# Optimization experiments

Measured on AMD Instinct MI355X. Metric: run time of the kernel, lower is better.

## Reference

```python
import jax, jax.numpy as jnp
import numpy as np

N = 100000; EI = 1600000; EC = 800000; G = 2000
FD = 512; H1 = 32; H2 = 32; EMB = 128; NH = 4
EPS = 1e-5


def setup_inputs() -> dict:
    key = jax.random.key(0)
    ks = jax.random.split(key, 30)
    p = lambda k, shp: (jax.random.normal(k, shp, jnp.float32) * 0.05)
    inp = {
        'feat': jax.random.normal(ks[0], (N, FD), jnp.float32),
        'inter_src': jax.random.randint(ks[1], (EI,), 0, N),
        'inter_dst': jax.random.randint(ks[2], (EI,), 0, N),
        'cross_src': jax.random.randint(ks[3], (EC,), 0, N),
        'cross_dst': jax.random.randint(ks[4], (EC,), 0, N),
        'graph_ids': jnp.sort(jax.random.randint(ks[5], (N,), 0, G)),
        # layer1
        'W_gc1': p(ks[6], (FD, NH * H1)), 'b_gc1': p(ks[7], (NH * H1,)),
        'W_gat1': p(ks[8], (FD, NH * H1)), 'al1': p(ks[9], (NH, H1)), 'ar1': p(ks[10], (NH, H1)), 'b_gat1': p(ks[11], (NH * H1,)),
        # layer2
        'W_gc2': p(ks[12], (NH * H1, NH * H2)), 'b_gc2': p(ks[13], (NH * H2,)),
        'W_gat2': p(ks[14], (NH * H1, NH * H2)), 'al2': p(ks[15], (NH, H2)), 'ar2': p(ks[16], (NH, H2)), 'b_gat2': p(ks[17], (NH * H2,)),
        # layer3
        'W_gc3': p(ks[18], (NH * H2, EMB)), 'b_gc3': p(ks[19], (EMB,)),
        'W_gat3': p(ks[20], (NH * H2, EMB)), 'al3': p(ks[21], (1, EMB)), 'ar3': p(ks[22], (1, EMB)), 'b_gat3': p(ks[23], (EMB,)),
        # batchnorms (gamma ones, beta zeros)
        'g1': jnp.ones((NH * H1,), jnp.float32), 'be1': jnp.zeros((NH * H1,), jnp.float32),
        'g2': jnp.ones((NH * H2,), jnp.float32), 'be2': jnp.zeros((NH * H2,), jnp.float32),
        'g3': jnp.ones((EMB,), jnp.float32), 'be3': jnp.zeros((EMB,), jnp.float32),
    }
    return inp


def _leaky(x):
    return jnp.where(x >= 0, x, 0.2 * x)


def _graph_conv(x, W, b, src, dst):
    # DGL GraphConv, norm='both': D_out^{-1/2} A D_in^{-1/2} X W + b (degrees clamped to >=1)
    ones = jnp.ones(src.shape[0], x.dtype)
    dout = jnp.clip(jax.ops.segment_sum(ones, src, num_segments=N), 1.0)
    din = jnp.clip(jax.ops.segment_sum(ones, dst, num_segments=N), 1.0)
    xw = (x @ W) * (dout ** -0.5)[:, None]          # project first (in >= out)
    agg = jax.ops.segment_sum(xw[src], dst, num_segments=N)
    return agg * (din ** -0.5)[:, None] + b


def _gat(x, W, al, ar, b, src, dst, H, d):
    # DGL GATConv: per-edge additive attention with edge softmax over incoming edges
    f = (x @ W).reshape(-1, H, d)                    # [N,H,d]
    el = jnp.sum(f * al, -1)                         # [N,H]
    er = jnp.sum(f * ar, -1)
    e = _leaky(el[src] + er[dst])                    # [E,H]
    m = jax.ops.segment_max(e, dst, num_segments=N)
    ex = jnp.exp(e - m[dst])
    s = jax.ops.segment_sum(ex, dst, num_segments=N)
    alpha = ex / s[dst]                              # [E,H]
    out = jax.ops.segment_sum(alpha[:, :, None] * f[src], dst, num_segments=N)
    return out + b.reshape(1, H, d), alpha


def _bn(x, g, b):
    mu = x.mean(0)
    v = jnp.mean((x - mu) ** 2, 0)
    return g * (x - mu) / jnp.sqrt(v + EPS) + b


def reference(feat, inter_src, inter_dst, cross_src, cross_dst, graph_ids,
              W_gc1, b_gc1, W_gat1, al1, ar1, b_gat1,
              W_gc2, b_gc2, W_gat2, al2, ar2, b_gat2,
              W_gc3, b_gc3, W_gat3, al3, ar3, b_gat3,
              g1, be1, g2, be2, g3, be3):
    h = feat
    hi = _graph_conv(h, W_gc1, b_gc1, inter_src, inter_dst)
    hc, _ = _gat(h, W_gat1, al1, ar1, b_gat1, cross_src, cross_dst, NH, H1)
    h = _bn(_leaky(hi + hc.reshape(N, -1)), g1, be1)
    hi = _graph_conv(h, W_gc2, b_gc2, inter_src, inter_dst)
    hc, _ = _gat(h, W_gat2, al2, ar2, b_gat2, cross_src, cross_dst, NH, H2)
    h = _bn(_leaky(hi + hc.reshape(N, -1)), g2, be2)
    h1 = _graph_conv(h, W_gc3, b_gc3, inter_src, inter_dst)
    h2, att = _gat(h, W_gat3, al3, ar3, b_gat3, cross_src, cross_dst, 1, EMB)
    h = _bn(h1 + h2[:, 0, :], g3, be3)
    att_sum = jax.ops.segment_sum(att[:, 0], cross_src, num_segments=N)   # [N]
    wh = h * att_sum[:, None]
    gsum = jax.ops.segment_sum(wh, graph_ids, num_segments=G)
    cnt = jnp.clip(jax.ops.segment_sum(jnp.ones(N, h.dtype), graph_ids, num_segments=G), 1.0)
    frag_embeddings = gsum / cnt[:, None]                                  # [G,EMB]
    return frag_embeddings, att_sum
```

## Files before the change

### kernel.cpp

```cpp
#include <hip/hip_runtime.h>
#include <math.h>

#define NN 100000
#define EIE 1600000
#define ECE 800000
#define GG 2000
#define FDIM 512
#define CC 128
#define BNEPS 1e-5f
#define SLOTI 48
#define SLOTC 32
#define FUSED_BLOCKS 3910

static inline int cdiv(long a, long b){ return (int)((a+b-1)/b); }

typedef __attribute__((ext_vector_type(8))) short short8;
typedef __attribute__((ext_vector_type(4))) float f32x4;

__device__ __forceinline__ unsigned short f2bf(float f){
  unsigned u = __float_as_uint(f);
  u += 0x7fffu + ((u >> 16) & 1u);
  return (unsigned short)(u >> 16);
}
__device__ __forceinline__ float bf2f(unsigned short h){
  return __uint_as_float(((unsigned)h) << 16);
}
__device__ __forceinline__ float2 ldbf2(const unsigned short* p){
  ushort2 u = *(const ushort2*)p;
  return make_float2(bf2f(u.x), bf2f(u.y));
}

__device__ __forceinline__ size_t wt_off(int n, int k) {
  return (size_t)(k >> 5)*8192 + (((n >> 4)*4 + ((k >> 3) & 3))*16 + (n & 15))*8 + (k & 7);
}
__global__ void k_pack_all(const float* __restrict__ Wgc1, const float* __restrict__ Wgat1,
                           const float* __restrict__ Wgc2, const float* __restrict__ Wgat2,
                           const float* __restrict__ Wgc3, const float* __restrict__ Wgat3,
                           unsigned short* __restrict__ Wth1, unsigned short* __restrict__ Wtl1,
                           unsigned short* __restrict__ Wth2, unsigned short* __restrict__ Wtl2,
                           unsigned short* __restrict__ Wth3, unsigned short* __restrict__ Wtl3) {
  int t = blockIdx.x*256 + threadIdx.x;
  const float *W1, *W2; unsigned short *oh, *ol; int FIN, tt;
  if (t < 131072)      { W1=Wgc1; W2=Wgat1; oh=Wth1; ol=Wtl1; FIN=512; tt=t; }
  else if (t < 163840) { W1=Wgc2; W2=Wgat2; oh=Wth2; ol=Wtl2; FIN=128; tt=t-131072; }
  else if (t < 196608) { W1=Wgc3; W2=Wgat3; oh=Wth3; ol=Wtl3; FIN=128; tt=t-163840; }
  else return;
  int n = tt / FIN, k = tt % FIN;
  float v = (n < 128) ? W1[(size_t)k*128 + n] : W2[(size_t)k*128 + (n-128)];
  unsigned short h = f2bf(v);
  size_t o = wt_off(n, k);
  oh[o] = h;
  ol[o] = f2bf(v - bf2f(h));
}

__global__ __launch_bounds__(512)
void k_fill_gemm1(const int* __restrict__ isrc, const int* __restrict__ idst,
                  const int* __restrict__ csrc, const int* __restrict__ cdst,
                  int* __restrict__ cnt_i, int* __restrict__ eid_i,
                  int* __restrict__ cnt_c, int* __restrict__ eid_c,
                  int* __restrict__ dout, float* __restrict__ att,
                  const float* __restrict__ xf,
                  const unsigned short* __restrict__ Bh, const unsigned short* __restrict__ Bl,
                  const float* __restrict__ al, const float* __restrict__ ar,
                  float* __restrict__ el, float* __restrict__ er,
                  unsigned short* __restrict__ Y1, unsigned short* __restrict__ Y2) {
  __shared__ __attribute__((aligned(16))) unsigned short sAh[4096];
  __shared__ __attribute__((aligned(16))) unsigned short sBh[8192];
  __shared__ __attribute__((aligned(16))) unsigned short sBl[8192];
  int r = blockIdx.x;
  int tid = threadIdx.x;

  if (r % 5 != 0) {
    int fi = r - 1 - (r-1)/5;
    int e = fi*512 + tid;
    if (e < EIE) {
      int d = idst[e];
      int p = atomicAdd(&cnt_i[d], 1);
      if (p < SLOTI) eid_i[d*SLOTI + p] = isrc[e];
      atomicAdd(&dout[isrc[e]], 1);
    }
    if (e < ECE) {
      int d = cdst[e];
      int p = atomicAdd(&cnt_c[d], 1);
      if (p < SLOTC) eid_c[d*SLOTC + p] = csrc[e];
    }
    if (e < NN) att[e] = 0.f;
    return;
  }

  int row0 = (r/5)*128;
  int lane = tid & 63, wid = tid >> 6;
  int wm = wid >> 2, wn = wid & 3;
  int l15 = lane & 15, quad = lane >> 4;

  f32x4 acc[4][4];
  #pragma unroll
  for (int mt = 0; mt < 4; ++mt)
    #pragma unroll
    for (int nt = 0; nt < 4; ++nt) acc[mt][nt] = (f32x4){0.f,0.f,0.f,0.f};

  for (int k0 = 0; k0 < FDIM; k0 += 32) {
    #pragma unroll
    for (int i = 0; i < 2; ++i) {
      int idx = tid + i*512;
      int rr = idx >> 3, c = idx & 7;
      int gr = row0 + rr; if (gr > NN-1) gr = NN-1;
      float4 v = *(const float4*)(xf + (size_t)gr*FDIM + k0 + c*4);
      ushort4 hh;
      hh.x = f2bf(v.x); hh.y = f2bf(v.y); hh.z = f2bf(v.z); hh.w = f2bf(v.w);
      *(ushort4*)&sAh[(((rr>>4)*4 + (c>>1))*16 + (rr&15))*8 + (c&1)*4] = hh;
    }
    const unsigned short* bhk = Bh + (size_t)k0*256;
    const unsigned short* blk = Bl + (size_t)k0*256;
    #pragma unroll
    for (int i = 0; i < 2; ++i) {
      int idx = tid + i*512;
      *(float4*)&sBh[idx*8] = *(const float4*)(bhk + idx*8);
      *(float4*)&sBl[idx*8] = *(const float4*)(blk + idx*8);
    }
    __syncthreads();
    short8 ah[4];
    #pragma unroll
    for (int mt = 0; mt < 4; ++mt)
      ah[mt] = *(const short8*)&sAh[(((wm*4+mt)*4 + quad)*16 + l15)*8];
    #pragma unroll
    for (int nt = 0; nt < 4; ++nt) {
      int off = (((wn*4+nt)*4 + quad)*16 + l15)*8;
      short8 bh = *(const short8*)&sBh[off];
      short8 bl = *(const short8*)&sBl[off];
      #pragma unroll
      for (int mt = 0; mt < 4; ++mt) {
        acc[mt][nt] = __builtin_amdgcn_mfma_f32_16x16x32_bf16(ah[mt], bh, acc[mt][nt], 0,0,0);
        acc[mt][nt] = __builtin_amdgcn_mfma_f32_16x16x32_bf16(ah[mt], bl, acc[mt][nt], 0,0,0);
      }
    }
    __syncthreads();
  }
  unsigned short* Y = (wn < 2) ? Y1 : Y2;
  int colbase = (wn & 1)*64;
  #pragma unroll
  for (int mt = 0; mt < 4; ++mt) {
    #pragma unroll
    for (int rr = 0; rr < 4; ++rr) {
      int row = row0 + (wm*4+mt)*16 + quad*4 + rr;
      if (row >= NN) continue;
      #pragma unroll
      for (int nt = 0; nt < 4; ++nt)
        Y[(size_t)row*CC + colbase + nt*16 + l15] = f2bf(acc[mt][nt][rr]);
    }
  }
  if (wn >= 2) {
    float alv[4], arv[4];
    #pragma unroll
    for (int nt = 0; nt < 4; ++nt) {
      int col = colbase + nt*16 + l15;
      alv[nt] = al[col]; arv[nt] = ar[col];
    }
    int hb = (wn & 1)*2;
    #pragma unroll
    for (int mt = 0; mt < 4; ++mt) {
      #pragma unroll
      for (int rr = 0; rr < 4; ++rr) {
        float pa0 = acc[mt][0][rr]*alv[0] + acc[mt][1][rr]*alv[1];
        float pb0 = acc[mt][0][rr]*arv[0] + acc[mt][1][rr]*arv[1];
        float pa1 = acc[mt][2][rr]*alv[2] + acc[mt][3][rr]*alv[3];
        float pb1 = acc[mt][2][rr]*arv[2] + acc[mt][3][rr]*arv[3];
        #pragma unroll
        for (int m = 1; m <= 8; m <<= 1) {
          pa0 += __shfl_xor(pa0, m); pb0 += __shfl_xor(pb0, m);
          pa1 += __shfl_xor(pa1, m); pb1 += __shfl_xor(pb1, m);
        }
        int row = row0 + (wm*4+mt)*16 + quad*4 + rr;
        if (l15 == 0 && row < NN) {
          el[(size_t)row*4 + hb]   = pa0;  er[(size_t)row*4 + hb]   = pb0;
          el[(size_t)row*4 + hb+1] = pa1;  er[(size_t)row*4 + hb+1] = pb1;
        }
      }
    }
  }
}

template<bool ELR>
__global__ __launch_bounds__(512)
void k_gemm2(const unsigned short* __restrict__ xb,
             const unsigned short* __restrict__ Bh, const unsigned short* __restrict__ Bl,
             const float* __restrict__ bnsc, const float* __restrict__ bnsh,
             const float* __restrict__ al, const float* __restrict__ ar,
             float* __restrict__ el, float* __restrict__ er,
             unsigned short* __restrict__ Y1, unsigned short* __restrict__ Y2) {
  __shared__ __attribute__((aligned(16))) unsigned short sAh[4096];
  __shared__ __attribute__((aligned(16))) unsigned short sBh[8192];
  __shared__ __attribute__((aligned(16))) unsigned short sBl[8192];
  int tid = threadIdx.x;
  int row0 = blockIdx.x*128;
  int lane = tid & 63, wid = tid >> 6;
  int wm = wid >> 2, wn = wid & 3;
  int l15 = lane & 15, quad = lane >> 4;

  f32x4 acc[4][4];
  #pragma unroll
  for (int mt = 0; mt < 4; ++mt)
    #pragma unroll
    for (int nt = 0; nt < 4; ++nt) acc[mt][nt] = (f32x4){0.f,0.f,0.f,0.f};

  for (int k0 = 0; k0 < CC; k0 += 32) {
    int rr = tid >> 2, c16 = tid & 3;
    int gr = row0 + rr; if (gr > NN-1) gr = NN-1;
    short8 u = *(const short8*)(xb + (size_t)gr*CC + k0 + c16*8);
    short8 o;
    #pragma unroll
    for (int j = 0; j < 8; ++j) {
      float f = bf2f((unsigned short)u[j]);
      f = f*bnsc[k0 + c16*8 + j] + bnsh[k0 + c16*8 + j];
      o[j] = (short)f2bf(f);
    }
    *(short8*)&sAh[(((rr>>4)*4 + c16)*16 + (rr&15))*8] = o;

    const unsigned short* bhk = Bh + (size_t)k0*256;
    const unsigned short* blk = Bl + (size_t)k0*256;
    #pragma unroll
    for (int i = 0; i < 2; ++i) {
      int idx = tid + i*512;
      *(float4*)&sBh[idx*8] = *(const float4*)(bhk + idx*8);
      *(float4*)&sBl[idx*8] = *(const float4*)(blk + idx*8);
    }
    __syncthreads();
    short8 ah[4];
    #pragma unroll
    for (int mt = 0; mt < 4; ++mt)
      ah[mt] = *(const short8*)&sAh[(((wm*4+mt)*4 + quad)*16 + l15)*8];
    #pragma unroll
    for (int nt = 0; nt < 4; ++nt) {
      int off = (((wn*4+nt)*4 + quad)*16 + l15)*8;
      short8 bh = *(const short8*)&sBh[off];
      short8 bl = *(const short8*)&sBl[off];
      #pragma unroll
      for (int mt = 0; mt < 4; ++mt) {
        acc[mt][nt] = __builtin_amdgcn_mfma_f32_16x16x32_bf16(ah[mt], bh, acc[mt][nt], 0,0,0);
        acc[mt][nt] = __builtin_amdgcn_mfma_f32_16x16x32_bf16(ah[mt], bl, acc[mt][nt], 0,0,0);
      }
    }
    __syncthreads();
  }
  unsigned short* Y = (wn < 2) ? Y1 : Y2;
  int colbase = (wn & 1)*64;
  #pragma unroll
  for (int mt = 0; mt < 4; ++mt) {
    #pragma unroll
    for (int rr = 0; rr < 4; ++rr) {
      int row = row0 + (wm*4+mt)*16 + quad*4 + rr;
      if (row >= NN) continue;
      #pragma unroll
      for (int nt = 0; nt < 4; ++nt)
        Y[(size_t)row*CC + colbase + nt*16 + l15] = f2bf(acc[mt][nt][rr]);
    }
  }
  if (ELR && wn >= 2) {
    float alv[4], arv[4];
    #pragma unroll
    for (int nt = 0; nt < 4; ++nt) {
      int col = colbase + nt*16 + l15;
      alv[nt] = al[col]; arv[nt] = ar[col];
    }
    int hb = (wn & 1)*2;
    #pragma unroll
    for (int mt = 0; mt < 4; ++mt) {
      #pragma unroll
      for (int rr = 0; rr < 4; ++rr) {
        float pa0 = acc[mt][0][rr]*alv[0] + acc[mt][1][rr]*alv[1];
        float pb0 = acc[mt][0][rr]*arv[0] + acc[mt][1][rr]*arv[1];
        float pa1 = acc[mt][2][rr]*alv[2] + acc[mt][3][rr]*alv[3];
        float pb1 = acc[mt][2][rr]*arv[2] + acc[mt][3][rr]*arv[3];
        #pragma unroll
        for (int m = 1; m <= 8; m <<= 1) {
          pa0 += __shfl_xor(pa0, m); pb0 += __shfl_xor(pb0, m);
          pa1 += __shfl_xor(pa1, m); pb1 += __shfl_xor(pb1, m);
        }
        int row = row0 + (wm*4+mt)*16 + quad*4 + rr;
        if (l15 == 0 && row < NN) {
          el[(size_t)row*4 + hb]   = pa0;  er[(size_t)row*4 + hb]   = pb0;
          el[(size_t)row*4 + hb+1] = pa1;  er[(size_t)row*4 + hb+1] = pb1;
        }
      }
    }
  }
}

template<int H>
__global__ __launch_bounds__(256)
void k_elr2(const unsigned short* __restrict__ f, const float* __restrict__ al,
            const float* __restrict__ ar, float* __restrict__ el, float* __restrict__ er,
            float* __restrict__ csq) {
  if (blockIdx.x == 0) csq[threadIdx.x] = 0.f;
  int lane = threadIdx.x & 63;
  int n = blockIdx.x*4 + (threadIdx.x >> 6);
  if (n >= NN) return;
  int c2 = lane*2;
  float2 v = ldbf2(f + (size_t)n*CC + c2);
  float2 a = *(const float2*)(al + c2);
  float2 b = *(const float2*)(ar + c2);
  float pa = v.x*a.x + v.y*a.y;
  float pb = v.x*b.x + v.y*b.y;
  const int W = (H == 1) ? 64 : 16;
  #pragma unroll
  for (int m = W>>1; m >= 1; m >>= 1) { pa += __shfl_xor(pa, m); pb += __shfl_xor(pb, m); }
  if ((lane & (W-1)) == 0) {
    int h = lane / W;
    el[(size_t)n*H + h] = pa;
    er[(size_t)n*H + h] = pb;
  }
}

template<int H, bool ATT, bool LEAKY>
__global__ __launch_bounds__(64)
void k_gather_fused(const unsigned short* __restrict__ A1, const unsigned short* __restrict__ A2,
                    const int* __restrict__ cnt_i, const int* __restrict__ eid_i,
                    const int* __restrict__ cnt_c, const int* __restrict__ eid_c,
                    const int* __restrict__ dout,
                    const float* __restrict__ el, const float* __restrict__ er,
                    const float* __restrict__ bgc, const float* __restrict__ bgat,
                    unsigned short* __restrict__ out, float* __restrict__ att) {
  int lane = threadIdx.x;
  int row = blockIdx.x;
  int grp = lane >> 4;
  int l4  = lane & 15;
  int c8  = l4*8;

  int deg = cnt_i[row];
  int lo = row*SLOTI, hi = lo + min(deg, SLOTI);
  float ax[8];
  #pragma unroll
  for (int k = 0; k < 8; ++k) ax[k] = 0.f;
  int j = lo + grp;
  for (; j + 4 < hi; j += 8) {
    int s0 = eid_i[j], s1 = eid_i[j+4];
    float d0 = rsqrtf((float)max(dout[s0], 1));
    float d1 = rsqrtf((float)max(dout[s1], 1));
    short8 u0 = *(const short8*)(A1 + (size_t)s0*CC + c8);
    short8 u1 = *(const short8*)(A1 + (size_t)s1*CC + c8);
    #pragma unroll
    for (int k = 0; k < 8; ++k)
      ax[k] += d0*bf2f((unsigned short)u0[k]) + d1*bf2f((unsigned short)u1[k]);
  }
  if (j < hi) {
    int s0 = eid_i[j];
    float d0 = rsqrtf((float)max(dout[s0], 1));
    short8 u0 = *(const short8*)(A1 + (size_t)s0*CC + c8);
    #pragma unroll
    for (int k = 0; k < 8; ++k) ax[k] += d0*bf2f((unsigned short)u0[k]);
  }
  float sc = rsqrtf((float)max(deg, 1));

  int h = (H == 1) ? 0 : (l4 >> 2);
  float erd = er[(size_t)row*H + h];
  int degc = cnt_c[row];
  int lo2 = row*SLOTC, hi2 = lo2 + min(degc, SLOTC);
  float gacc[8];
  #pragma unroll
  for (int k = 0; k < 8; ++k) gacc[k] = 0.f;
  float denom = 0.f;
  j = lo2 + grp;
  for (; j + 4 < hi2; j += 8) {
    int s0 = eid_c[j], s1 = eid_c[j+4];
    float v0 = el[(size_t)s0*H + h] + erd;
    float v1 = el[(size_t)s1*H + h] + erd;
    v0 = (v0 >= 0.f) ? v0 : 0.2f*v0;
    v1 = (v1 >= 0.f) ? v1 : 0.2f*v1;
    float w0 = __expf(v0), w1 = __expf(v1);
    denom += w0 + w1;
    short8 u0 = *(const short8*)(A2 + (size_t)s0*CC + c8);
    short8 u1 = *(const short8*)(A2 + (size_t)s1*CC + c8);
    #pragma unroll
    for (int k = 0; k < 8; ++k)
      gacc[k] += w0*bf2f((unsigned short)u0[k]) + w1*bf2f((unsigned short)u1[k]);
  }
  if (j < hi2) {
    int s = eid_c[j];
    float v = el[(size_t)s*H + h] + erd;
    v = (v >= 0.f) ? v : 0.2f*v;
    float w = __expf(v);
    denom += w;
    short8 u = *(const short8*)(A2 + (size_t)s*CC + c8);
    #pragma unroll
    for (int k = 0; k < 8; ++k) gacc[k] += w * bf2f((unsigned short)u[k]);
  }

  #pragma unroll
  for (int m = 16; m <= 32; m <<= 1) {
    denom += __shfl_xor(denom, m);
    #pragma unroll
    for (int k = 0; k < 8; ++k) {
      ax[k]   += __shfl_xor(ax[k], m);
      gacc[k] += __shfl_xor(gacc[k], m);
    }
  }
  float inv = (denom > 0.f) ? 1.0f/denom : 0.f;

  if (ATT) {
    for (j = lo2 + grp; j < hi2; j += 4) {
      int s = eid_c[j];
      if (l4 == 0) {
        float v = el[(size_t)s*H] + erd;
        v = (v >= 0.f) ? v : 0.2f*v;
        atomicAdd(&att[s], __expf(v)*inv);
      }
    }
  }

  if (grp == 0) {
    float4 b1a = *(const float4*)(bgc + c8);
    float4 b1b = *(const float4*)(bgc + c8 + 4);
    float4 b2a = *(const float4*)(bgat + c8);
    float4 b2b = *(const float4*)(bgat + c8 + 4);
    float bb1[8] = {b1a.x,b1a.y,b1a.z,b1a.w,b1b.x,b1b.y,b1b.z,b1b.w};
    float bb2[8] = {b2a.x,b2a.y,b2a.z,b2a.w,b2b.x,b2b.y,b2b.z,b2b.w};
    short8 ov;
    #pragma unroll
    for (int k = 0; k < 8; ++k) {
      float o = ax[k]*sc + bb1[k] + gacc[k]*inv + bb2[k];
      if (LEAKY) o = (o >= 0.f) ? o : 0.2f*o;
      ov[k] = (short)f2bf(o);
    }
    *(short8*)(out + (size_t)row*CC + c8) = ov;
  }
}

__global__ __launch_bounds__(256)
void k_bn_stats(const unsigned short* __restrict__ t, float* __restrict__ csq) {
  __shared__ float red[4][128];
  int lane = threadIdx.x & 63, g = threadIdx.x >> 6;
  int c2 = lane*2;
  float s0=0.f, s1=0.f, q0=0.f, q1=0.f;
  for (int r = blockIdx.x*4 + g; r < NN; r += gridDim.x*4) {
    float2 v = ldbf2(t + (size_t)r*CC + c2);
    s0 += v.x; s1 += v.y; q0 += v.x*v.x; q1 += v.y*v.y;
  }
  red[g][c2] = s0; red[g][c2+1] = s1;
  __syncthreads();
  if (threadIdx.x < 128) {
    float a = red[0][threadIdx.x] + red[1][threadIdx.x] + red[2][threadIdx.x] + red[3][threadIdx.x];
    atomicAdd(&csq[threadIdx.x], a);
  }
  __syncthreads();
  red[g][c2] = q0; red[g][c2+1] = q1;
  __syncthreads();
  if (threadIdx.x < 128) {
    float a = red[0][threadIdx.x] + red[1][threadIdx.x] + red[2][threadIdx.x] + red[3][threadIdx.x];
    atomicAdd(&csq[128 + threadIdx.x], a);
  }
}

__global__ void k_bn_coef(const float* __restrict__ csqc, float* __restrict__ csq,
                          const float* __restrict__ g, const float* __restrict__ be,
                          float* __restrict__ sc, float* __restrict__ sh) {
  int c = threadIdx.x;
  float sv = csqc[c], qv = csqc[128+c];
  float mu = sv * (1.f/NN);
  float var = qv * (1.f/NN) - mu*mu;
  float r = rsqrtf(var + BNEPS);
  float s = g[c]*r;
  sc[c] = s;
  sh[c] = be[c] - s*mu;
  csq[c] = 0.f; csq[128+c] = 0.f;
}

__global__ void k_pool_bn(const unsigned short* __restrict__ t, const float* __restrict__ att,
                          const int* __restrict__ gids, const float* __restrict__ bnsc,
                          const float* __restrict__ bnsh, float* __restrict__ frag) {
  int g = blockIdx.x;
  __shared__ int se[2];
  if (threadIdx.x < 2) {
    int target = g + threadIdx.x;
    int lo = 0, hi = NN;
    while (lo < hi) { int mid = (lo + hi) >> 1; if (gids[mid] < target) lo = mid + 1; else hi = mid; }
    se[threadIdx.x] = lo;
  }
  __syncthreads();
  int lo = se[0], hi = se[1];
  int col = threadIdx.x;
  float scv = bnsc[col], shv = bnsh[col];
  float acc = 0.f;
  for (int n = lo; n < hi; ++n) acc += (bf2f(t[(size_t)n*CC + col])*scv + shv) * att[n];
  frag[(size_t)g*CC + col] = acc / (float)max(hi - lo, 1);
}

extern "C" void kernel_launch(void* const* d_in, const int* in_sizes, int n_in,
                              void* d_out, int out_size, void* d_ws, size_t ws_size,
                              hipStream_t stream) {
  const float* feat  = (const float*)d_in[0];
  const int* isrc    = (const int*)d_in[1];
  const int* idst    = (const int*)d_in[2];
  const int* csrc    = (const int*)d_in[3];
  const int* cdst    = (const int*)d_in[4];
  const int* gids    = (const int*)d_in[5];
  const float* W_gc1 = (const float*)d_in[6];  const float* b_gc1 = (const float*)d_in[7];
  const float* W_gat1= (const float*)d_in[8];  const float* al1   = (const float*)d_in[9];
  const float* ar1   = (const float*)d_in[10]; const float* b_gat1= (const float*)d_in[11];
  const float* W_gc2 = (const float*)d_in[12]; const float* b_gc2 = (const float*)d_in[13];
  const float* W_gat2= (const float*)d_in[14]; const float* al2   = (const float*)d_in[15];
  const float* ar2   = (const float*)d_in[16]; const float* b_gat2= (const float*)d_in[17];
  const float* W_gc3 = (const float*)d_in[18]; const float* b_gc3 = (const float*)d_in[19];
  const float* W_gat3= (const float*)d_in[20]; const float* al3   = (const float*)d_in[21];
  const float* ar3   = (const float*)d_in[22]; const float* b_gat3= (const float*)d_in[23];
  const float* g1 = (const float*)d_in[24]; const float* be1 = (const float*)d_in[25];
  const float* g2 = (const float*)d_in[26]; const float* be2 = (const float*)d_in[27];
  const float* g3 = (const float*)d_in[28]; const float* be3 = (const float*)d_in[29];

  const size_t NC = (size_t)NN*CC;
  float* el   = (float*)d_ws;
  float* er   = el + (size_t)NN*4;
  float* csq  = er + (size_t)NN*4;
  float* bnsc = csq + 256;
  float* bnsh = bnsc + CC;
  unsigned short* B  = (unsigned short*)(bnsh + CC);
  unsigned short* A1 = B + NC;
  unsigned short* A2 = A1 + NC;
  unsigned short* Wth1 = A2 + NC;
  unsigned short* Wtl1 = Wth1 + 256*FDIM;
  unsigned short* Wth2 = Wtl1 + 256*FDIM;
  unsigned short* Wtl2 = Wth2 + 256*CC;
  unsigned short* Wth3 = Wtl2 + 256*CC;
  unsigned short* Wtl3 = Wth3 + 256*CC;
  int* cnt_i  = (int*)(Wtl3 + 256*CC);
  int* cnt_c  = cnt_i + NN;
  int* dout   = cnt_c + NN;
  int* eid_i  = dout + NN;
  int* eid_c  = eid_i + (size_t)NN*SLOTI;

  float* frag = (float*)d_out;
  float* att  = frag + (size_t)GG*CC;

  hipMemsetAsync(cnt_i, 0, 3*(size_t)NN*sizeof(int), stream);
  hipMemsetAsync(csq, 0, 256*sizeof(float), stream);
  k_pack_all<<<cdiv(196608,256), 256, 0, stream>>>(W_gc1, W_gat1, W_gc2, W_gat2, W_gc3, W_gat3,
                                                   Wth1, Wtl1, Wth2, Wtl2, Wth3, Wtl3);
  k_fill_gemm1<<<FUSED_BLOCKS, 512, 0, stream>>>(isrc, idst, csrc, cdst,
                                                 cnt_i, eid_i, cnt_c, eid_c, dout, att,
                                                 feat, Wth1, Wtl1, al1, ar1, el, er, A1, A2);

  k_gather_fused<4,false,true><<<NN, 64, 0, stream>>>(A1, A2, cnt_i, eid_i,
                                                      cnt_c, eid_c, dout, el, er,
                                                      b_gc1, b_gat1, B, nullptr);
  k_bn_stats<<<256, 256, 0, stream>>>(B, csq);
  k_bn_coef<<<1, 128, 0, stream>>>(csq, csq, g1, be1, bnsc, bnsh);

  k_gemm2<true><<<cdiv(NN,128), 512, 0, stream>>>(B, Wth2, Wtl2, bnsc, bnsh,
                                                  al2, ar2, el, er, A1, A2);
  k_gather_fused<4,false,true><<<NN, 64, 0, stream>>>(A1, A2, cnt_i, eid_i,
                                                      cnt_c, eid_c, dout, el, er,
                                                      b_gc2, b_gat2, B, nullptr);
  k_bn_stats<<<256, 256, 0, stream>>>(B, csq);
  k_bn_coef<<<1, 128, 0, stream>>>(csq, csq, g2, be2, bnsc, bnsh);

  k_gemm2<false><<<cdiv(NN,128), 512, 0, stream>>>(B, Wth3, Wtl3, bnsc, bnsh,
                                                   nullptr, nullptr, nullptr, nullptr, A1, A2);
  k_elr2<1><<<cdiv(NN,4), 256, 0, stream>>>(A2, al3, ar3, el, er, csq);
  k_gather_fused<1,true,false><<<NN, 64, 0, stream>>>(A1, A2, cnt_i, eid_i,
                                                      cnt_c, eid_c, dout, el, er,
                                                      b_gc3, b_gat3, B, att);
  k_bn_stats<<<256, 256, 0, stream>>>(B, csq);
  k_bn_coef<<<1, 128, 0, stream>>>(csq, csq, g3, be3, bnsc, bnsh);

  k_pool_bn<<<GG, 128, 0, stream>>>(B, att, gids, bnsc, bnsh, frag);
}
```

Before: 1.011 ms.

## Fuse BN coef, dout scaling and layer-3 attention logits into gemm2

The batchnorm coefficient computation moves into each gemm2 block's prologue, so two k_bn_coef launches go away; separate stats buffers replace the per-layer zeroing. The source-degree normalisation is applied once per row in the gemm2 epilogue rather than per edge in the gather, which removes a random dout load and rsqrt per edge in layers 2 and 3. The layer-3 el/er logits are computed from the accumulators inside gemm2, which eliminates the k_elr2 kernel and its re-read of A2. Each gemm2 block now redundantly computes the BN coefficients, and the epilogue does slightly more work.

```diff
diff --git a/kernel.cpp b/kernel.cpp
--- a/kernel.cpp
+++ b/kernel.cpp
@@ -180,23 +180,36 @@
   }
 }
 
-template<bool ELR>
+template<bool ELR4, bool ELR1>
 __global__ __launch_bounds__(512)
 void k_gemm2(const unsigned short* __restrict__ xb,
              const unsigned short* __restrict__ Bh, const unsigned short* __restrict__ Bl,
-             const float* __restrict__ bnsc, const float* __restrict__ bnsh,
+             const float* __restrict__ csqin, const float* __restrict__ g,
+             const float* __restrict__ be, const int* __restrict__ dout,
              const float* __restrict__ al, const float* __restrict__ ar,
              float* __restrict__ el, float* __restrict__ er,
              unsigned short* __restrict__ Y1, unsigned short* __restrict__ Y2) {
   __shared__ __attribute__((aligned(16))) unsigned short sAh[4096];
   __shared__ __attribute__((aligned(16))) unsigned short sBh[8192];
   __shared__ __attribute__((aligned(16))) unsigned short sBl[8192];
+  __shared__ float sSC[CC], sSH[CC];
   int tid = threadIdx.x;
   int row0 = blockIdx.x*128;
   int lane = tid & 63, wid = tid >> 6;
   int wm = wid >> 2, wn = wid & 3;
   int l15 = lane & 15, quad = lane >> 4;
 
+  if (tid < CC) {
+    float sv = csqin[tid], qv = csqin[CC + tid];
+    float mu = sv * (1.f/NN);
+    float var = qv * (1.f/NN) - mu*mu;
+    float rn = rsqrtf(var + BNEPS);
+    float s = g[tid]*rn;
+    sSC[tid] = s;
+    sSH[tid] = be[tid] - s*mu;
+  }
+  __syncthreads();
+
   f32x4 acc[4][4];
   #pragma unroll
   for (int mt = 0; mt < 4; ++mt)
@@ -211,7 +224,7 @@
     #pragma unroll
     for (int j = 0; j < 8; ++j) {
       float f = bf2f((unsigned short)u[j]);
-      f = f*bnsc[k0 + c16*8 + j] + bnsh[k0 + c16*8 + j];
+      f = f*sSC[k0 + c16*8 + j] + sSH[k0 + c16*8 + j];
       o[j] = (short)f2bf(f);
     }
     *(short8*)&sAh[(((rr>>4)*4 + c16)*16 + (rr&15))*8] = o;
@@ -250,68 +263,81 @@
     for (int rr = 0; rr < 4; ++rr) {
       int row = row0 + (wm*4+mt)*16 + quad*4 + rr;
       if (row >= NN) continue;
+      float scv = (wn < 2) ? rsqrtf((float)max(dout[row], 1)) : 1.0f;
       #pragma unroll
       for (int nt = 0; nt < 4; ++nt)
-        Y[(size_t)row*CC + colbase + nt*16 + l15] = f2bf(acc[mt][nt][rr]);
-    }
-  }
-  if (ELR && wn >= 2) {
-    float alv[4], arv[4];
-    #pragma unroll
-    for (int nt = 0; nt < 4; ++nt) {
-      int col = colbase + nt*16 + l15;
-      alv[nt] = al[col]; arv[nt] = ar[col];
-    }
-    int hb = (wn & 1)*2;
-    #pragma unroll
-    for (int mt = 0; mt < 4; ++mt) {
-      #pragma unroll
-      for (int rr = 0; rr < 4; ++rr) {
-        float pa0 = acc[mt][0][rr]*alv[0] + acc[mt][1][rr]*alv[1];
-        float pb0 = acc[mt][0][rr]*arv[0] + acc[mt][1][rr]*arv[1];
-        float pa1 = acc[mt][2][rr]*alv[2] + acc[mt][3][rr]*alv[3];
-        float pb1 = acc[mt][2][rr]*arv[2] + acc[mt][3][rr]*arv[3];
+        Y[(size_t)row*CC + colbase + nt*16 + l15] = f2bf(acc[mt][nt][rr]*scv);
+    }
+  }
+  if constexpr (ELR4) {
+    if (wn >= 2) {
+      float alv[4], arv[4];
+      #pragma unroll
+      for (int nt = 0; nt < 4; ++nt) {
+        int col = colbase + nt*16 + l15;
+        alv[nt] = al[col]; arv[nt] = ar[col];
+      }
+      int hb = (wn & 1)*2;
+      #pragma unroll
+      for (int mt = 0; mt < 4; ++mt) {
         #pragma unroll
-        for (int m = 1; m <= 8; m <<= 1) {
-          pa0 += __shfl_xor(pa0, m); pb0 += __shfl_xor(pb0, m);
-          pa1 += __shfl_xor(pa1, m); pb1 += __shfl_xor(pb1, m);
+        for (int rr = 0; rr < 4; ++rr) {
+          float pa0 = acc[mt][0][rr]*alv[0] + acc[mt][1][rr]*alv[1];
+          float pb0 = acc[mt][0][rr]*arv[0] + acc[mt][1][rr]*arv[1];
+          float pa1 = acc[mt][2][rr]*alv[2] + acc[mt][3][rr]*alv[3];
+          float pb1 = acc[mt][2][rr]*arv[2] + acc[mt][3][rr]*arv[3];
+          #pragma unroll
+          for (int m = 1; m <= 8; m <<= 1) {
+            pa0 += __shfl_xor(pa0, m); pb0 += __shfl_xor(pb0, m);
+            pa1 += __shfl_xor(pa1, m); pb1 += __shfl_xor(pb1, m);
+          }
+          int row = row0 + (wm*4+mt)*16 + quad*4 + rr;
+          if (l15 == 0 && row < NN) {
+            el[(size_t)row*4 + hb]   = pa0;  er[(size_t)row*4 + hb]   = pb0;
+            el[(size_t)row*4 + hb+1] = pa1;  er[(size_t)row*4 + hb+1] = pb1;
+          }
         }
-        int row = row0 + (wm*4+mt)*16 + quad*4 + rr;
-        if (l15 == 0 && row < NN) {
-          el[(size_t)row*4 + hb]   = pa0;  er[(size_t)row*4 + hb]   = pb0;
-          el[(size_t)row*4 + hb+1] = pa1;  er[(size_t)row*4 + hb+1] = pb1;
+      }
+    }
+  }
+  if constexpr (ELR1) {
+    __shared__ float sE[2][2][CC];
+    if (wn >= 2) {
+      float alv[4], arv[4];
+      #pragma unroll
+      for (int nt = 0; nt < 4; ++nt) {
+        int col = colbase + nt*16 + l15;
+        alv[nt] = al[col]; arv[nt] = ar[col];
+      }
+      #pragma unroll
+      for (int mt = 0; mt < 4; ++mt) {
+        #pragma unroll
+        for (int rr = 0; rr < 4; ++rr) {
+          float pa = acc[mt][0][rr]*alv[0] + acc[mt][1][rr]*alv[1]
+                   + acc[mt][2][rr]*alv[2] + acc[mt][3][rr]*alv[3];
+          float pb = acc[mt][0][rr]*arv[0] + acc[mt][1][rr]*arv[1]
+                   + acc[mt][2][rr]*arv[2] + acc[mt][3][rr]*arv[3];
+          #pragma unroll
+          for (int m = 1; m <= 8; m <<= 1) {
+            pa += __shfl_xor(pa, m); pb += __shfl_xor(pb, m);
+          }
+          int rowl = (wm*4+mt)*16 + quad*4 + rr;
+          if (l15 == 0) { sE[0][wn-2][rowl] = pa; sE[1][wn-2][rowl] = pb; }
         }
       }
     }
-  }
-}
-
-template<int H>
-__global__ __launch_bounds__(256)
-void k_elr2(const unsigned short* __restrict__ f, const float* __restrict__ al,
-            const float* __restrict__ ar, float* __restrict__ el, float* __restrict__ er,
-            float* __restrict__ csq) {
-  if (blockIdx.x == 0) csq[threadIdx.x] = 0.f;
-  int lane = threadIdx.x & 63;
-  int n = blockIdx.x*4 + (threadIdx.x >> 6);
-  if (n >= NN) return;
-  int c2 = lane*2;
-  float2 v = ldbf2(f + (size_t)n*CC + c2);
-  float2 a = *(const float2*)(al + c2);
-  float2 b = *(const float2*)(ar + c2);
-  float pa = v.x*a.x + v.y*a.y;
-  float pb = v.x*b.x + v.y*b.y;
-  const int W = (H == 1) ? 64 : 16;
-  #pragma unroll
-  for (int m = W>>1; m >= 1; m >>= 1) { pa += __shfl_xor(pa, m); pb += __shfl_xor(pb, m); }
-  if ((lane & (W-1)) == 0) {
-    int h = lane / W;
-    el[(size_t)n*H + h] = pa;
-    er[(size_t)n*H + h] = pb;
-  }
-}
-
-template<int H, bool ATT, bool LEAKY>
+    __syncthreads();
+    if (tid < CC) {
+      int row = row0 + tid;
+      if (row < NN) {
+        el[row] = sE[0][0][tid] + sE[0][1][tid];
+        er[row] = sE[1][0][tid] + sE[1][1][tid];
+      }
+    }
+  }
+}
+
+template<int H, bool DSC, bool ATT, bool LEAKY>
 __global__ __launch_bounds__(64)
 void k_gather_fused(const unsigned short* __restrict__ A1, const unsigned short* __restrict__ A2,
                     const int* __restrict__ cnt_i, const int* __restrict__ eid_i,
@@ -334,20 +360,25 @@
   int j = lo + grp;
   for (; j + 4 < hi; j += 8) {
     int s0 = eid_i[j], s1 = eid_i[j+4];
-    float d0 = rsqrtf((float)max(dout[s0], 1));
-    float d1 = rsqrtf((float)max(dout[s1], 1));
+    float d0 = DSC ? rsqrtf((float)max(dout[s0], 1)) : 1.0f;
+    float d1 = DSC ? rsqrtf((float)max(dout[s1], 1)) : 1.0f;
     short8 u0 = *(const short8*)(A1 + (size_t)s0*CC + c8);
     short8 u1 = *(const short8*)(A1 + (size_t)s1*CC + c8);
     #pragma unroll
-    for (int k = 0; k < 8; ++k)
-      ax[k] += d0*bf2f((unsigned short)u0[k]) + d1*bf2f((unsigned short)u1[k]);
+    for (int k = 0; k < 8; ++k) {
+      if (DSC) ax[k] += d0*bf2f((unsigned short)u0[k]) + d1*bf2f((unsigned short)u1[k]);
+      else     ax[k] += bf2f((unsigned short)u0[k]) + bf2f((unsigned short)u1[k]);
+    }
   }
   if (j < hi) {
     int s0 = eid_i[j];
-    float d0 = rsqrtf((float)max(dout[s0], 1));
+    float d0 = DSC ? rsqrtf((float)max(dout[s0], 1)) : 1.0f;
     short8 u0 = *(const short8*)(A1 + (size_t)s0*CC + c8);
     #pragma unroll
-    for (int k = 0; k < 8; ++k) ax[k] += d0*bf2f((unsigned short)u0[k]);
+    for (int k = 0; k < 8; ++k) {
+      if (DSC) ax[k] += d0*bf2f((unsigned short)u0[k]);
+      else     ax[k] += bf2f((unsigned short)u0[k]);
+    }
   }
   float sc = rsqrtf((float)max(deg, 1));
 
@@ -450,18 +481,16 @@
   }
 }
 
-__global__ void k_bn_coef(const float* __restrict__ csqc, float* __restrict__ csq,
+__global__ void k_bn_coef(const float* __restrict__ csqc,
                           const float* __restrict__ g, const float* __restrict__ be,
                           float* __restrict__ sc, float* __restrict__ sh) {
   int c = threadIdx.x;
-  float sv = csqc[c], qv = csqc[128+c];
-  float mu = sv * (1.f/NN);
-  float var = qv * (1.f/NN) - mu*mu;
+  float mu = csqc[c] * (1.f/NN);
+  float var = csqc[128+c] * (1.f/NN) - mu*mu;
   float r = rsqrtf(var + BNEPS);
   float s = g[c]*r;
   sc[c] = s;
   sh[c] = be[c] - s*mu;
-  csq[c] = 0.f; csq[128+c] = 0.f;
 }
 
 __global__ void k_pool_bn(const unsigned short* __restrict__ t, const float* __restrict__ att,
@@ -510,7 +539,7 @@
   float* el   = (float*)d_ws;
   float* er   = el + (size_t)NN*4;
   float* csq  = er + (size_t)NN*4;
-  float* bnsc = csq + 256;
+  float* bnsc = csq + 768;
   float* bnsh = bnsc + CC;
   unsigned short* B  = (unsigned short*)(bnsh + CC);
   unsigned short* A1 = B + NC;
@@ -531,35 +560,32 @@
   float* att  = frag + (size_t)GG*CC;
 
   hipMemsetAsync(cnt_i, 0, 3*(size_t)NN*sizeof(int), stream);
-  hipMemsetAsync(csq, 0, 256*sizeof(float), stream);
+  hipMemsetAsync(csq, 0, 768*sizeof(float), stream);
   k_pack_all<<<cdiv(196608,256), 256, 0, stream>>>(W_gc1, W_gat1, W_gc2, W_gat2, W_gc3, W_gat3,
                                                    Wth1, Wtl1, Wth2, Wtl2, Wth3, Wtl3);
   k_fill_gemm1<<<FUSED_BLOCKS, 512, 0, stream>>>(isrc, idst, csrc, cdst,
                                                  cnt_i, eid_i, cnt_c, eid_c, dout, att,
                                                  feat, Wth1, Wtl1, al1, ar1, el, er, A1, A2);
 
-  k_gather_fused<4,false,true><<<NN, 64, 0, stream>>>(A1, A2, cnt_i, eid_i,
-                                                      cnt_c, eid_c, dout, el, er,
-                                                      b_gc1, b_gat1, B, nullptr);
+  k_gather_fused<4,true,false,true><<<NN, 64, 0, stream>>>(A1, A2, cnt_i, eid_i,
+                                                           cnt_c, eid_c, dout, el, er,
+                                                           b_gc1, b_gat1, B, nullptr);
   k_bn_stats<<<256, 256, 0, stream>>>(B, csq);
-  k_bn_coef<<<1, 128, 0, stream>>>(csq, csq, g1, be1, bnsc, bnsh);
-
-  k_gemm2<true><<<cdiv(NN,128), 512, 0, stream>>>(B, Wth2, Wtl2, bnsc, bnsh,
-                                                  al2, ar2, el, er, A1, A2);
-  k_gather_fused<4,false,true><<<NN, 64, 0, stream>>>(A1, A2, cnt_i, eid_i,
-                                                      cnt_c, eid_c, dout, el, er,
-                                                      b_gc2, b_gat2, B, nullptr);
-  k_bn_stats<<<256, 256, 0, stream>>>(B, csq);
-  k_bn_coef<<<1, 128, 0, stream>>>(csq, csq, g2, be2, bnsc, bnsh);
-
-  k_gemm2<false><<<cdiv(NN,128), 512, 0, stream>>>(B, Wth3, Wtl3, bnsc, bnsh,
-                                                   nullptr, nullptr, nullptr, nullptr, A1, A2);
-  k_elr2<1><<<cdiv(NN,4), 256, 0, stream>>>(A2, al3, ar3, el, er, csq);
-  k_gather_fused<1,true,false><<<NN, 64, 0, stream>>>(A1, A2, cnt_i, eid_i,
-                                                      cnt_c, eid_c, dout, el, er,
-                                                      b_gc3, b_gat3, B, att);
-  k_bn_stats<<<256, 256, 0, stream>>>(B, csq);
-  k_bn_coef<<<1, 128, 0, stream>>>(csq, csq, g3, be3, bnsc, bnsh);
+
+  k_gemm2<true,false><<<cdiv(NN,128), 512, 0, stream>>>(B, Wth2, Wtl2, csq, g1, be1, dout,
+                                                        al2, ar2, el, er, A1, A2);
+  k_gather_fused<4,false,false,true><<<NN, 64, 0, stream>>>(A1, A2, cnt_i, eid_i,
+                                                            cnt_c, eid_c, dout, el, er,
+                                                            b_gc2, b_gat2, B, nullptr);
+  k_bn_stats<<<256, 256, 0, stream>>>(B, csq + 256);
+
+  k_gemm2<false,true><<<cdiv(NN,128), 512, 0, stream>>>(B, Wth3, Wtl3, csq + 256, g2, be2, dout,
+                                                        al3, ar3, el, er, A1, A2);
+  k_gather_fused<1,false,true,false><<<NN, 64, 0, stream>>>(A1, A2, cnt_i, eid_i,
+                                                            cnt_c, eid_c, dout, el, er,
+                                                            b_gc3, b_gat3, B, att);
+  k_bn_stats<<<256, 256, 0, stream>>>(B, csq + 512);
+  k_bn_coef<<<1, 128, 0, stream>>>(csq + 512, g3, be3, bnsc, bnsh);
 
   k_pool_bn<<<GG, 128, 0, stream>>>(B, att, gids, bnsc, bnsh, frag);
 }
```

Result: no change. 997.7 us (-1.3%).
